# Kernel optimization log

Hardware: AMD Instinct MI355X
Metric: run time of the kernel (lower is better)

The kernel has to match this reference:

```python
import jax, jax.numpy as jnp
import numpy as np
import math
from jax import lax

A_BICUBIC = -0.75  # PyTorch bicubic coefficient


def _bicubic_resize_matrix(out_n, in_n):
    """Dense [out_n, in_n] matrix implementing 1D bicubic resize (half-pixel,
    align_corners=False, border-replicated taps) exactly like F.interpolate."""
    a = A_BICUBIC
    src = (np.arange(out_n) + 0.5) * (in_n / out_n) - 0.5
    i0 = np.floor(src).astype(np.int64)
    t = src - i0
    M = np.zeros((out_n, in_n), dtype=np.float32)
    for k in range(-1, 3):
        idx = np.clip(i0 + k, 0, in_n - 1)
        d = np.abs(t - k)
        w = np.where(d <= 1.0, (a + 2) * d**3 - (a + 3) * d**2 + 1.0,
                     np.where(d < 2.0, a * d**3 - 5 * a * d**2 + 8 * a * d - 4 * a, 0.0))
        np.add.at(M, (np.arange(out_n), idx), w)
    return jnp.asarray(M)


def _relative_position_index(w):
    coords = np.stack(np.meshgrid(np.arange(w), np.arange(w), indexing='ij'))  # [2,w,w]
    cf = coords.reshape(2, -1)
    rel = (cf[:, :, None] - cf[:, None, :]).transpose(1, 2, 0)  # [w^2,w^2,2]
    rel[..., 0] += w - 1
    rel[..., 1] += w - 1
    rel[..., 0] *= 2 * w - 1
    return rel.sum(-1)  # [w^2, w^2]


def _grid_sample_bilinear(img, grid):
    """img: [G,d,Hi,Wi]; grid: [G,Ho,Wo,2] (x,y) in [-1,1].
    Bilinear, padding_mode='zeros', align_corners=False."""
    G, d, Hi, Wi = img.shape
    Ho, Wo = grid.shape[1:3]
    gx = (grid[..., 0] + 1.0) * (Wi * 0.5) - 0.5
    gy = (grid[..., 1] + 1.0) * (Hi * 0.5) - 0.5
    x0 = jnp.floor(gx)
    y0 = jnp.floor(gy)
    imgf = img.reshape(G, d, Hi * Wi)
    out = jnp.zeros((G, d, Ho * Wo), img.dtype)
    for dy in (0, 1):
        for dx in (0, 1):
            xi = x0 + dx
            yi = y0 + dy
            w = (1.0 - jnp.abs(gx - xi)) * (1.0 - jnp.abs(gy - yi))
            valid = (xi >= 0) & (xi < Wi) & (yi >= 0) & (yi < Hi)
            xic = jnp.clip(xi, 0, Wi - 1).astype(jnp.int32)
            yic = jnp.clip(yi, 0, Hi - 1).astype(jnp.int32)
            flat = (yic * Wi + xic).reshape(G, 1, Ho * Wo)
            v = jnp.take_along_axis(imgf, flat, axis=2)  # [G,d,HoWo]
            out = out + v * (w * valid).reshape(G, 1, Ho * Wo)
    return out.reshape(G, d, Ho, Wo)


def deformable_attention(x, q_w, q_b, k_w, k_b, v_w, v_b, o_w, o_b, dw_w, dw_b, off_w, bias_table, offset_scale=2.0):
    B, N, C = x.shape
    H = W = int(math.sqrt(N))
    heads = off_w.shape[0] // 2
    hd = C // heads
    wsz = (int(math.isqrt(bias_table.shape[0])) + 1) // 2  # (2w-1)^2 -> w

    xi = x.reshape(B, H, W, C).transpose(0, 3, 1, 2)  # [B,C,H,W]

    def conv1x1(t, w, b=None):
        y = jnp.einsum('bchw,oc->bohw', t, w)
        return y if b is None else y + b[None, :, None, None]

    Q = conv1x1(xi, q_w, q_b)
    K = conv1x1(xi, k_w, k_b)
    V = conv1x1(xi, v_w, v_b)

    # offset network: depthwise 5x5 conv -> GELU -> 1x1 -> tanh -> *scale
    h = lax.conv_general_dilated(xi, dw_w, (1, 1), 'SAME', feature_group_count=C,
                                 dimension_numbers=('NCHW', 'OIHW', 'NCHW'))
    h = jax.nn.gelu(h + dw_b[None, :, None, None], approximate=False)
    offsets = jnp.tanh(conv1x1(h, off_w)) * offset_scale  # [B,2*heads,H,W]
    offsets = offsets.reshape(B, heads, 2, H, W).transpose(0, 1, 3, 4, 2)  # [B,n,H,W,2]

    gy, gx = jnp.meshgrid(jnp.linspace(-1.0, 1.0, H), jnp.linspace(-1.0, 1.0, W), indexing='ij')
    grid = jnp.stack((gx, gy), axis=-1)  # [H,W,2]
    samp = jnp.clip(grid[None, None] + offsets, -1.0, 1.0).reshape(B * heads, H, W, 2)

    Kh = K.reshape(B * heads, hd, H, W)
    Vh = V.reshape(B * heads, hd, H, W)
    Ks = _grid_sample_bilinear(Kh, samp).reshape(B, heads, hd, N).transpose(0, 1, 3, 2)  # [B,n,N,d]
    Vs = _grid_sample_bilinear(Vh, samp).reshape(B, heads, hd, N).transpose(0, 1, 3, 2)
    Qh = Q.reshape(B, heads, hd, N).transpose(0, 1, 3, 2)  # [B,n,N,d]

    scores = jnp.einsum('bhid,bhjd->bhij', Qh, Ks) / math.sqrt(hd)

    # relative bias: table lookup on static index, bicubic upsample w^2 -> N
    rpi = _relative_position_index(wsz)  # static numpy [w^2,w^2]
    bias0 = bias_table[jnp.asarray(rpi.reshape(-1)), 0].reshape(wsz * wsz, wsz * wsz)
    M = _bicubic_resize_matrix(N, wsz * wsz)
    bias = M @ bias0 @ M.T  # [N,N]
    scores = scores + bias[None, None]

    probs = jax.nn.softmax(scores, axis=-1)
    out = jnp.einsum('bhij,bhjd->bhid', probs, Vs)  # [B,n,N,d]
    out = out.transpose(0, 1, 3, 2).reshape(B, C, H, W)  # b (h d) p q
    out = conv1x1(out, o_w, o_b)
    return out.reshape(B, C, N).transpose(0, 2, 1)  # [B,N,C]


def setup_inputs() -> dict:
    key = jax.random.key(0)
    ks = jax.random.split(key, 16)
    B, N, C = 4, 1024, 512
    heads, wsz, kk = 8, 8, 5
    s = 0.02
    return {
        'x': jax.random.normal(ks[0], (B, N, C), jnp.float32),
        'q_w': jax.random.normal(ks[1], (C, C), jnp.float32) * s,
        'q_b': jax.random.normal(ks[2], (C,), jnp.float32) * s,
        'k_w': jax.random.normal(ks[3], (C, C), jnp.float32) * s,
        'k_b': jax.random.normal(ks[4], (C,), jnp.float32) * s,
        'v_w': jax.random.normal(ks[5], (C, C), jnp.float32) * s,
        'v_b': jax.random.normal(ks[6], (C,), jnp.float32) * s,
        'o_w': jax.random.normal(ks[7], (C, C), jnp.float32) * s,
        'o_b': jax.random.normal(ks[8], (C,), jnp.float32) * s,
        'dw_w': jax.random.normal(ks[9], (C, 1, kk, kk), jnp.float32) * s,
        'dw_b': jax.random.normal(ks[10], (C,), jnp.float32) * s,
        'off_w': jax.random.normal(ks[11], (2 * heads, C), jnp.float32) * s,
        'bias_table': jax.random.normal(ks[12], ((2 * wsz - 1) ** 2, 1), jnp.float32),
    }


def reference(x, q_w, q_b, k_w, k_b, v_w, v_b, o_w, o_b, dw_w, dw_b, off_w, bias_table):
    return deformable_attention(x, q_w, q_b, k_w, k_b, v_w, v_b, o_w, o_b, dw_w, dw_b, off_w, bias_table)
```

## Files before the change

### kernel.cpp

```cpp
#include <hip/hip_runtime.h>
#include <math.h>

typedef unsigned short ushort;
typedef __attribute__((ext_vector_type(8))) short bf16x8;
typedef __attribute__((ext_vector_type(4))) float f32x4;

#define MFMA16(a, b, c) __builtin_amdgcn_mfma_f32_16x16x32_bf16(a, b, c, 0, 0, 0)
#define GLOAD16(g, l)                                                   \
  __builtin_amdgcn_global_load_lds(                                     \
      (const __attribute__((address_space(1))) unsigned int*)(g),       \
      (__attribute__((address_space(3))) unsigned int*)(l), 16, 0, 0)

__device__ __forceinline__ ushort f2bf(float f) {
  unsigned u = __float_as_uint(f);
  u += 0x7FFFu + ((u >> 16) & 1u);
  return (ushort)(u >> 16);
}
__device__ __forceinline__ float bf2f(ushort b) {
  return __uint_as_float(((unsigned)b) << 16);
}
__device__ __forceinline__ unsigned pk_bf16(float a, float b) {
  unsigned u;
  asm("v_cvt_pk_bf16_f32 %0, %1, %2" : "=v"(u) : "v"(a), "v"(b));
  return u;
}

__device__ __forceinline__ void bicubic_taps(int i, float* w, int* idx) {
  const float a = -0.75f;
  float src = ((float)i + 0.5f) * 0.0625f - 0.5f;
  float fi = floorf(src);
  int i0 = (int)fi;
  float t = src - fi;
  #pragma unroll
  for (int k = -1; k <= 2; ++k) {
    float d = fabsf(t - (float)k);
    float wv;
    if (d <= 1.0f)
      wv = ((a + 2.0f) * d - (a + 3.0f)) * d * d + 1.0f;
    else if (d < 2.0f)
      wv = a * (((d - 5.0f) * d + 8.0f) * d - 4.0f);
    else
      wv = 0.0f;
    int ic = i0 + k;
    ic = ic < 0 ? 0 : (ic > 63 ? 63 : ic);
    w[k + 1] = wv;
    idx[k + 1] = ic;
  }
}

__global__ __launch_bounds__(256) void stage1(
    const float* __restrict__ x, const float* __restrict__ q_w,
    const float* __restrict__ k_w, const float* __restrict__ v_w,
    const float* __restrict__ o_w, const float* __restrict__ dw_w,
    const float* __restrict__ dw_b, const float* __restrict__ off_w,
    const float* __restrict__ btab, ushort* __restrict__ Xh,
    ushort* __restrict__ Wq, ushort* __restrict__ Wk, ushort* __restrict__ Wv,
    ushort* __restrict__ Woh, ushort* __restrict__ Wol,
    float* __restrict__ samp, ushort* __restrict__ biasb) {
  __shared__ float smem[16768];
  int blk = blockIdx.x;
  int tid = threadIdx.x;

  if (blk < 1024) {
    float* tab = smem;
    int i = blk;
    if (tid < 225) tab[tid] = btab[tid];
    __syncthreads();
    float wA[4]; int iA[4];
    bicubic_taps(i, wA, iA);
    for (int j = tid; j < 1024; j += 256) {
      float wB[4]; int iB[4];
      bicubic_taps(j, wB, iB);
      float sum = 0.f;
      #pragma unroll
      for (int ka = 0; ka < 4; ++ka) {
        int pa = iA[ka];
        int py = pa >> 3, px = pa & 7;
        float wa = wA[ka];
        #pragma unroll
        for (int kb = 0; kb < 4; ++kb) {
          int qb = iB[kb];
          int qy = qb >> 3, qx = qb & 7;
          sum += wa * wB[kb] * tab[(py - qy + 7) * 15 + (px - qx + 7)];
        }
      }
      biasb[(size_t)i * 1024 + j] = f2bf(sum);
    }
  } else if (blk < 1280) {
    float* wT = smem;
    float* hT = smem + 8256;
    float* ofs = smem + 16512;
    int ob = blk - 1024;
    int x0 = (ob & 1) * 16;
    int y = (ob >> 1) & 31;
    int b = ob >> 6;

    for (int e = tid; e < 2048; e += 256) {
      int o = e >> 7, c4 = e & 127;
      *(float4*)&wT[o * 516 + c4 * 4] = *(const float4*)&off_w[o * 512 + c4 * 4];
    }

    int c = tid * 2;
    float2 dwv[25];
    #pragma unroll
    for (int k = 0; k < 25; ++k) {
      dwv[k].x = dw_w[(size_t)c * 25 + k];
      dwv[k].y = dw_w[(size_t)(c + 1) * 25 + k];
    }
    float2 cb = *(const float2*)&dw_b[c];

    const float* xb = x + (size_t)b * 1024 * 512 + c;
    bool rv[5];
    #pragma unroll
    for (int r = 0; r < 5; ++r) {
      int yy = y - 2 + r;
      rv[r] = (yy >= 0 && yy < 32);
    }
    float2 win[5][5];
    #pragma unroll
    for (int j = 0; j < 4; ++j) {
      int xc = x0 - 2 + j;
      bool cvld = (xc >= 0 && xc < 32);
      #pragma unroll
      for (int r = 0; r < 5; ++r) {
        win[r][j] = (rv[r] && cvld)
            ? *(const float2*)&xb[(size_t)((y - 2 + r) * 32 + xc) * 512]
            : make_float2(0.f, 0.f);
      }
    }
    #pragma unroll
    for (int i = 0; i < 16; ++i) {
      int xc = x0 + i + 2;
      bool cvld = (xc < 32);
      #pragma unroll
      for (int r = 0; r < 5; ++r) {
        win[r][4] = (rv[r] && cvld)
            ? *(const float2*)&xb[(size_t)((y - 2 + r) * 32 + xc) * 512]
            : make_float2(0.f, 0.f);
      }
      float sx = cb.x, sy = cb.y;
      #pragma unroll
      for (int r = 0; r < 5; ++r)
        #pragma unroll
        for (int j = 0; j < 5; ++j) {
          sx += win[r][j].x * dwv[r * 5 + j].x;
          sy += win[r][j].y * dwv[r * 5 + j].y;
        }
      float g0 = 0.5f * sx * (1.0f + erff(sx * 0.70710678118654752f));
      float g1 = 0.5f * sy * (1.0f + erff(sy * 0.70710678118654752f));
      *(float2*)&hT[i * 516 + c] = make_float2(g0, g1);
      #pragma unroll
      for (int r = 0; r < 5; ++r) {
        win[r][0] = win[r][1]; win[r][1] = win[r][2];
        win[r][2] = win[r][3]; win[r][3] = win[r][4];
      }
    }
    __syncthreads();
    {
      int o = tid & 15, px = tid >> 4;
      float acc = 0.f;
      #pragma unroll 4
      for (int c4 = 0; c4 < 128; ++c4) {
        float4 hv = *(const float4*)&hT[px * 516 + c4 * 4];
        float4 wv = *(const float4*)&wT[o * 516 + c4 * 4];
        acc += hv.x * wv.x + hv.y * wv.y + hv.z * wv.z + hv.w * wv.w;
      }
      ofs[px * 16 + o] = tanhf(acc) * 2.0f;
    }
    __syncthreads();
    if (tid < 128) {
      int px = tid >> 3, h = tid & 7;
      int n = y * 32 + x0 + px;
      float gx = -1.0f + 2.0f * (float)(x0 + px) / 31.0f;
      float gy = -1.0f + 2.0f * (float)y / 31.0f;
      float sx = fminf(fmaxf(gx + ofs[px * 16 + 2 * h], -1.0f), 1.0f);
      float sy = fminf(fmaxf(gy + ofs[px * 16 + 2 * h + 1], -1.0f), 1.0f);
      float2 pc;
      pc.x = (sx + 1.0f) * 16.0f - 0.5f;
      pc.y = (sy + 1.0f) * 16.0f - 0.5f;
      ((float2*)samp)[(size_t)(b * 8 + h) * 1024 + n] = pc;
    }
  } else if (blk < 3328) {
    int i = (blk - 1280) * 256 + tid;
    float4 v = ((const float4*)x)[i];
    ushort4 h;
    h.x = f2bf(v.x); h.y = f2bf(v.y); h.z = f2bf(v.z); h.w = f2bf(v.w);
    ((ushort4*)Xh)[i] = h;
  } else {
    int blk2 = blk - 3328;
    int grp = blk2 >> 8;
    int i = (blk2 & 255) * 256 + tid;
    if (grp < 3) {
      const float* in = grp == 0 ? q_w : grp == 1 ? k_w : v_w;
      ushort* hi = grp == 0 ? Wq : grp == 1 ? Wk : Wv;
      float4 v = ((const float4*)in)[i];
      ushort4 h;
      h.x = f2bf(v.x); h.y = f2bf(v.y); h.z = f2bf(v.z); h.w = f2bf(v.w);
      ((ushort4*)hi)[i] = h;
    } else {
      float4 v = ((const float4*)o_w)[i];
      ushort4 h, l;
      h.x = f2bf(v.x); l.x = f2bf(v.x - bf2f(h.x));
      h.y = f2bf(v.y); l.y = f2bf(v.y - bf2f(h.y));
      h.z = f2bf(v.z); l.z = f2bf(v.z - bf2f(h.z));
      h.w = f2bf(v.w); l.w = f2bf(v.w - bf2f(h.w));
      ((ushort4*)Woh)[i] = h;
      ((ushort4*)Wol)[i] = l;
    }
  }
}

__global__ __launch_bounds__(256) void gemm_qkv(
    const ushort* __restrict__ X, const ushort* __restrict__ Wq,
    const ushort* __restrict__ Wk, const ushort* __restrict__ Wv,
    const float* __restrict__ b0, const float* __restrict__ b1,
    const float* __restrict__ b2, ushort* __restrict__ Qo,
    ushort* __restrict__ Ko, ushort* __restrict__ Vo) {
  __shared__ ushort lds[12288];
  ushort* sA = lds;
  ushort* sB = lds + 8192;
  int which = blockIdx.x >> 3;
  int n0 = (blockIdx.x & 7) * 64;
  int m0 = blockIdx.y * 128;
  const ushort* W; const float* bb; ushort* Y; float scale;
  if (which == 0)      { W = Wq; bb = b0; Y = Qo; scale = 0.125f; }
  else if (which == 1) { W = Wk; bb = b1; Y = Ko; scale = 1.0f; }
  else                 { W = Wv; bb = b2; Y = Vo; scale = 1.0f; }

  int tid = threadIdx.x;
  int lane = tid & 63;
  int w = tid >> 6;
  int wr = (w >> 1) * 64;
  int wc = (w & 1) * 32;
  int l8r = lane >> 3;
  int sll = ((lane & 7) ^ l8r) << 3;
  int l16 = lane & 15, lq = lane >> 4;

  f32x4 acc[4][2];
  f32x4 zero = {0.f, 0.f, 0.f, 0.f};
  #pragma unroll
  for (int m = 0; m < 4; ++m)
    #pragma unroll
    for (int n = 0; n < 2; ++n) acc[m][n] = zero;

  for (int kt = 0; kt < 8; ++kt) {
    int kk = kt * 64;
    __syncthreads();
    #pragma unroll
    for (int q = 0; q < 4; ++q) {
      int ci = w * 4 + q;
      GLOAD16(X + (size_t)(m0 + ci * 8 + l8r) * 512 + kk + sll, sA + ci * 512);
    }
    #pragma unroll
    for (int q = 0; q < 2; ++q) {
      int ci = w * 2 + q;
      GLOAD16(W + (size_t)(n0 + ci * 8 + l8r) * 512 + kk + sll, sB + ci * 512);
    }
    __syncthreads();
    #pragma unroll
    for (int ks = 0; ks < 2; ++ks) {
      int slot = ks * 4 + lq;
      bf16x8 a[4], bvv[2];
      #pragma unroll
      for (int m = 0; m < 4; ++m) {
        int r = wr + m * 16 + l16;
        a[m] = *(const bf16x8*)&sA[r * 64 + ((slot ^ (r & 7)) << 3)];
      }
      #pragma unroll
      for (int n = 0; n < 2; ++n) {
        int r = wc + n * 16 + l16;
        bvv[n] = *(const bf16x8*)&sB[r * 64 + ((slot ^ (r & 7)) << 3)];
      }
      #pragma unroll
      for (int m = 0; m < 4; ++m)
        #pragma unroll
        for (int n = 0; n < 2; ++n)
          acc[m][n] = MFMA16(a[m], bvv[n], acc[m][n]);
    }
  }
  #pragma unroll
  for (int n = 0; n < 2; ++n) {
    int col = n0 + wc + n * 16 + l16;
    float bv = bb[col];
    #pragma unroll
    for (int m = 0; m < 4; ++m) {
      #pragma unroll
      for (int j = 0; j < 4; ++j) {
        int row = m0 + wr + m * 16 + lq * 4 + j;
        Y[(size_t)row * 512 + col] = f2bf((acc[m][n][j] + bv) * scale);
      }
    }
  }
}

__global__ __launch_bounds__(256) void gemm_o(
    const ushort* __restrict__ A, const ushort* __restrict__ Wh,
    const ushort* __restrict__ Wl, const float* __restrict__ bias,
    float* __restrict__ Y) {
  __shared__ ushort sA[4096];
  __shared__ ushort sWh[4096];
  __shared__ ushort sWl[4096];
  int m0 = blockIdx.y * 64, n0 = blockIdx.x * 64;
  int tid = threadIdx.x;
  int lane = tid & 63;
  int w = tid >> 6;
  int wr = (w >> 1) * 32;
  int wc = (w & 1) * 32;
  int l8r = lane >> 3;
  int sll = ((lane & 7) ^ l8r) << 3;
  int l16 = lane & 15, lq = lane >> 4;

  f32x4 acc[2][2];
  f32x4 zero = {0.f, 0.f, 0.f, 0.f};
  #pragma unroll
  for (int m = 0; m < 2; ++m)
    #pragma unroll
    for (int n = 0; n < 2; ++n) acc[m][n] = zero;

  for (int kt = 0; kt < 8; ++kt) {
    int kk = kt * 64;
    __syncthreads();
    #pragma unroll
    for (int q = 0; q < 2; ++q) {
      int ci = w * 2 + q;
      size_t ga = (size_t)(m0 + ci * 8 + l8r) * 512 + kk + sll;
      GLOAD16(A + ga, sA + ci * 512);
      size_t gw = (size_t)(n0 + ci * 8 + l8r) * 512 + kk + sll;
      GLOAD16(Wh + gw, sWh + ci * 512);
      GLOAD16(Wl + gw, sWl + ci * 512);
    }
    __syncthreads();
    #pragma unroll
    for (int ks = 0; ks < 2; ++ks) {
      int slot = ks * 4 + lq;
      bf16x8 a[2], bh[2], bl[2];
      #pragma unroll
      for (int m = 0; m < 2; ++m) {
        int r = wr + m * 16 + l16;
        a[m] = *(const bf16x8*)&sA[r * 64 + ((slot ^ (r & 7)) << 3)];
      }
      #pragma unroll
      for (int n = 0; n < 2; ++n) {
        int r = wc + n * 16 + l16;
        int ph = (slot ^ (r & 7)) << 3;
        bh[n] = *(const bf16x8*)&sWh[r * 64 + ph];
        bl[n] = *(const bf16x8*)&sWl[r * 64 + ph];
      }
      #pragma unroll
      for (int m = 0; m < 2; ++m)
        #pragma unroll
        for (int n = 0; n < 2; ++n) {
          acc[m][n] = MFMA16(a[m], bh[n], acc[m][n]);
          acc[m][n] = MFMA16(a[m], bl[n], acc[m][n]);
        }
    }
  }
  #pragma unroll
  for (int n = 0; n < 2; ++n) {
    int col = n0 + wc + n * 16 + l16;
    float bv = bias[col];
    #pragma unroll
    for (int m = 0; m < 2; ++m) {
      #pragma unroll
      for (int j = 0; j < 4; ++j) {
        int row = m0 + wr + m * 16 + lq * 4 + j;
        Y[(size_t)row * 512 + col] = acc[m][n][j] + bv;
      }
    }
  }
}

__global__ __launch_bounds__(256) void grid_sample(
    const ushort* __restrict__ K, const ushort* __restrict__ V,
    const float* __restrict__ samp, ushort* __restrict__ Ks,
    ushort* __restrict__ Vt) {
  __shared__ ushort sV[64][72];
  int bh = blockIdx.y;
  int b = bh >> 3, h = bh & 7;
  int jb = blockIdx.x;
  int d = threadIdx.x & 63;
  for (int p = 0; p < 16; ++p) {
    int jl = p * 4 + (threadIdx.x >> 6);
    int j = jb * 64 + jl;
    float2 pc = ((const float2*)samp)[(size_t)bh * 1024 + j];
    float gx = pc.x, gy = pc.y;
    float x0 = floorf(gx), y0 = floorf(gy);
    float aK = 0.f, aV = 0.f;
    #pragma unroll
    for (int dy = 0; dy < 2; ++dy)
      #pragma unroll
      for (int dx = 0; dx < 2; ++dx) {
        float xi = x0 + (float)dx, yi = y0 + (float)dy;
        float wgt = (1.0f - fabsf(gx - xi)) * (1.0f - fabsf(gy - yi));
        if (xi >= 0.f && xi < 32.f && yi >= 0.f && yi < 32.f) {
          size_t base = ((size_t)b * 1024 + (int)yi * 32 + (int)xi) * 512 + h * 64 + d;
          aK += bf2f(K[base]) * wgt;
          aV += bf2f(V[base]) * wgt;
        }
      }
    Ks[((size_t)bh * 1024 + j) * 64 + d] = f2bf(aK);
    sV[jl][d] = f2bf(aV);
  }
  __syncthreads();
  int dd = threadIdx.x >> 2, c4 = threadIdx.x & 3;
  bf16x8 v0, v1;
  #pragma unroll
  for (int k = 0; k < 8; ++k) v0[k] = (short)sV[c4 * 16 + k][dd];
  #pragma unroll
  for (int k = 0; k < 8; ++k) v1[k] = (short)sV[c4 * 16 + 8 + k][dd];
  size_t o = ((size_t)bh * 64 + dd) * 1024 + jb * 64 + c4 * 16;
  *(bf16x8*)&Vt[o] = v0;
  *(bf16x8*)&Vt[o + 8] = v1;
}

__global__ __launch_bounds__(512, 6) void attn_mfma(
    const ushort* __restrict__ Qh, const ushort* __restrict__ Ks,
    const ushort* __restrict__ Vt, const ushort* __restrict__ bias,
    ushort* __restrict__ Oh) {
  __shared__ ushort sK[2][2][2048];
  __shared__ ushort sVt[2][2][2048];
  __shared__ ushort sP[8][640];

  int tid = threadIdx.x;
  int lane = tid & 63;
  int w = tid >> 6;
  int qg = w & 3;
  int kvh = w >> 2;
  int l16 = lane & 15, lq = lane >> 4;
  int blk = blockIdx.x;
  int xcd = blk & 7;
  int rr = blk >> 3;
  int bh = ((rr & 3) << 3) + xcd;
  int i0 = (rr >> 2) * 64;
  int b = bh >> 3, h = bh & 7;

  bf16x8 qh[2];
  #pragma unroll
  for (int s = 0; s < 2; ++s)
    qh[s] = *(const bf16x8*)&Qh[((size_t)b * 1024 + i0 + qg * 16 + l16) * 512 +
                                h * 64 + s * 32 + lq * 8];

  f32x4 oacc[4];
  f32x4 zero = {0.f, 0.f, 0.f, 0.f};
  #pragma unroll
  for (int n = 0; n < 4; ++n) oacc[n] = zero;
  float mq = -INFINITY, lsum = 0.f;

  ushort* myP = sP[w];
  int krow = qg * 8 + (lane >> 3);
  int kslot = (lane & 7) ^ (krow & 7);
  int vrow = qg * 16 + (lane >> 2);
  int vslot = (lane & 3) ^ (vrow & 3);
  size_t kbase = ((size_t)bh * 1024 + kvh * 512 + krow) * 64 + kslot * 8;
  size_t vbase = ((size_t)bh * 64 + vrow) * 1024 + kvh * 512 + vslot * 8;
  ushort* dK0 = &sK[0][kvh][qg * 8 * 64];  ushort* dK1 = &sK[1][kvh][qg * 8 * 64];
  ushort* dV0 = &sVt[0][kvh][qg * 16 * 32]; ushort* dV1 = &sVt[1][kvh][qg * 16 * 32];
  const ushort* bprow = bias + (size_t)(i0 + qg * 16 + l16) * 1024 + kvh * 512;

  GLOAD16(Ks + kbase, dK0);
  GLOAD16(Vt + vbase, dV0);
  ushort4 bias_c[2];
  #pragma unroll
  for (int n = 0; n < 2; ++n)
    bias_c[n] = *(const ushort4*)&bprow[n * 16 + lq * 4];
  __syncthreads();

  int cur = 0;
  for (int t = 0; t < 16; ++t) {
    if (t < 15) {
      size_t off = (size_t)(t + 1) * 32;
      GLOAD16(Ks + kbase + off * 64, cur ? dK0 : dK1);
      GLOAD16(Vt + vbase + off, cur ? dV0 : dV1);
    }
    f32x4 sacc[2];
    #pragma unroll
    for (int n = 0; n < 2; ++n) {
      sacc[n][0] = bf2f(bias_c[n].x);
      sacc[n][1] = bf2f(bias_c[n].y);
      sacc[n][2] = bf2f(bias_c[n].z);
      sacc[n][3] = bf2f(bias_c[n].w);
    }
    if (t < 15) {
      #pragma unroll
      for (int n = 0; n < 2; ++n)
        bias_c[n] = *(const ushort4*)&bprow[(t + 1) * 32 + n * 16 + lq * 4];
    }
    const ushort* k_t = sK[cur][kvh];
    __builtin_amdgcn_s_setprio(1);
    #pragma unroll
    for (int ks = 0; ks < 2; ++ks) {
      int cslot = ((ks * 4 + lq) ^ (l16 & 7)) * 8;
      #pragma unroll
      for (int n = 0; n < 2; ++n) {
        bf16x8 aK = *(const bf16x8*)&k_t[(n * 16 + l16) * 64 + cslot];
        sacc[n] = MFMA16(aK, qh[ks], sacc[n]);
      }
    }
    __builtin_amdgcn_s_setprio(0);
    float mt = fmaxf(fmaxf(fmaxf(sacc[0][0], sacc[0][1]), fmaxf(sacc[0][2], sacc[0][3])),
                     fmaxf(fmaxf(sacc[1][0], sacc[1][1]), fmaxf(sacc[1][2], sacc[1][3])));
    mt = fmaxf(mt, __shfl_xor(mt, 16));
    mt = fmaxf(mt, __shfl_xor(mt, 32));
    if (!__all(mt <= mq + 8.0f)) {
      float mn = fmaxf(mq, mt);
      float sc = __expf(mq - mn);
      mq = mn;
      lsum *= sc;
      float scq[4];
      #pragma unroll
      for (int r = 0; r < 4; ++r) scq[r] = __shfl(sc, lq * 4 + r);
      #pragma unroll
      for (int n = 0; n < 4; ++n)
        #pragma unroll
        for (int r = 0; r < 4; ++r) oacc[n][r] *= scq[r];
    }
    float ts = 0.f;
    #pragma unroll
    for (int n = 0; n < 2; ++n) {
      float p0 = __expf(sacc[n][0] - mq);
      float p1 = __expf(sacc[n][1] - mq);
      float p2 = __expf(sacc[n][2] - mq);
      float p3 = __expf(sacc[n][3] - mq);
      ts += (p0 + p1) + (p2 + p3);
      uint2 u = make_uint2(pk_bf16(p0, p1), pk_bf16(p2, p3));
      *(uint2*)&myP[l16 * 40 + n * 16 + lq * 4] = u;
    }
    ts += __shfl_xor(ts, 16);
    ts += __shfl_xor(ts, 32);
    lsum += ts;
    bf16x8 pa = *(const bf16x8*)&myP[l16 * 40 + lq * 8];
    const ushort* vt_t = sVt[cur][kvh];
    __builtin_amdgcn_s_setprio(1);
    #pragma unroll
    for (int n = 0; n < 4; ++n) {
      int row = n * 16 + l16;
      bf16x8 bv = *(const bf16x8*)&vt_t[row * 32 + ((lq ^ (row & 3)) * 8)];
      oacc[n] = MFMA16(pa, bv, oacc[n]);
    }
    __builtin_amdgcn_s_setprio(0);
    __syncthreads();
    cur ^= 1;
  }

  float* mO = (float*)sK;
  float* mML = (float*)sVt;
  if (w >= 4) {
    int base = ((w - 4) * 64 + lane) * 16;
    #pragma unroll
    for (int n = 0; n < 4; ++n)
      #pragma unroll
      for (int r = 0; r < 4; ++r) mO[base + n * 4 + r] = oacc[n][r];
    mML[((w - 4) * 64 + lane) * 2 + 0] = mq;
    mML[((w - 4) * 64 + lane) * 2 + 1] = lsum;
  }
  __syncthreads();
  if (w < 4) {
    float mB = mML[(w * 64 + lane) * 2 + 0];
    float lB = mML[(w * 64 + lane) * 2 + 1];
    float mS = fmaxf(mq, mB);
    float fA = __expf(mq - mS), fB = __expf(mB - mS);
    float linv = 1.0f / (lsum * fA + lB * fB);
    float cAv = fA * linv, cBv = fB * linv;
    float cA[4], cB[4];
    #pragma unroll
    for (int r = 0; r < 4; ++r) {
      cA[r] = __shfl(cAv, lq * 4 + r);
      cB[r] = __shfl(cBv, lq * 4 + r);
    }
    int base = (w * 64 + lane) * 16;
    #pragma unroll
    for (int r = 0; r < 4; ++r) {
      int qr = i0 + qg * 16 + lq * 4 + r;
      #pragma unroll
      for (int n = 0; n < 4; ++n) {
        float v = oacc[n][r] * cA[r] + mO[base + n * 4 + r] * cB[r];
        size_t o = ((size_t)b * 1024 + qr) * 512 + h * 64 + n * 16 + l16;
        Oh[o] = f2bf(v);
      }
    }
  }
}

extern "C" void kernel_launch(void* const* d_in, const int* in_sizes, int n_in,
                              void* d_out, int out_size, void* d_ws, size_t ws_size,
                              hipStream_t stream) {
  const float* x     = (const float*)d_in[0];
  const float* q_w   = (const float*)d_in[1];
  const float* q_b   = (const float*)d_in[2];
  const float* k_w   = (const float*)d_in[3];
  const float* k_b   = (const float*)d_in[4];
  const float* v_w   = (const float*)d_in[5];
  const float* v_b   = (const float*)d_in[6];
  const float* o_w   = (const float*)d_in[7];
  const float* o_b   = (const float*)d_in[8];
  const float* dw_w  = (const float*)d_in[9];
  const float* dw_b  = (const float*)d_in[10];
  const float* off_w = (const float*)d_in[11];
  const float* btab  = (const float*)d_in[12];

  float* ws = (float*)d_ws;
  const size_t SZ = (size_t)4 * 1024 * 512;
  float* samp = ws;

  ushort* u = (ushort*)(samp + 65536);
  ushort* Xh    = u;
  ushort* Qb    = Xh + SZ;
  ushort* Kb    = Qb + SZ;
  ushort* Vb    = Kb + SZ;
  ushort* Ksb   = Vb + SZ;
  ushort* Vtr   = Ksb + SZ;
  ushort* Aoh   = Vtr + SZ;
  ushort* biasb = Aoh + SZ;
  ushort* Wq    = biasb + 1048576;
  ushort* Wk    = Wq + 262144;
  ushort* Wv    = Wk + 262144;
  ushort* Woh   = Wv + 262144;
  ushort* Wol   = Woh + 262144;

  stage1<<<4352, 256, 0, stream>>>(x, q_w, k_w, v_w, o_w, dw_w, dw_b, off_w,
                                   btab, Xh, Wq, Wk, Wv, Woh, Wol, samp, biasb);

  gemm_qkv<<<dim3(24, 32), 256, 0, stream>>>(Xh, Wq, Wk, Wv, q_b, k_b, v_b,
                                             Qb, Kb, Vb);

  grid_sample<<<dim3(16, 32), 256, 0, stream>>>(Kb, Vb, samp, Ksb, Vtr);

  attn_mfma<<<512, 512, 0, stream>>>(Qb, Ksb, Vtr, biasb, Aoh);

  gemm_o<<<dim3(8, 64), 256, 0, stream>>>(Aoh, Woh, Wol, o_b, (float*)d_out);
}
```

Measured before the change: 103.6 us.

## Load attention K/V fragments directly from global and widen QKV GEMM tiles

The attention kernel drops the double-buffered LDS staging of K and V^T. Each wave now loads its MFMA operand fragments straight from global memory into registers, which removes the per-iteration block barrier and the LDS traffic. The loop is unrolled by four and the launch-bounds occupancy hint is lowered from six to four. Separately, the QKV GEMM moves to 512-thread blocks with 128x128 tiles, halving the grid and cutting redundant X loads. The risks are uncoalesced, duplicated global or L2 reads for K/V across query-group waves and fewer resident waves.

```diff
diff --git a/kernel.cpp b/kernel.cpp
--- a/kernel.cpp
+++ b/kernel.cpp
@@ -210,17 +210,17 @@
   }
 }
 
-__global__ __launch_bounds__(256) void gemm_qkv(
+__global__ __launch_bounds__(512) void gemm_qkv(
     const ushort* __restrict__ X, const ushort* __restrict__ Wq,
     const ushort* __restrict__ Wk, const ushort* __restrict__ Wv,
     const float* __restrict__ b0, const float* __restrict__ b1,
     const float* __restrict__ b2, ushort* __restrict__ Qo,
     ushort* __restrict__ Ko, ushort* __restrict__ Vo) {
-  __shared__ ushort lds[12288];
+  __shared__ ushort lds[16384];
   ushort* sA = lds;
   ushort* sB = lds + 8192;
-  int which = blockIdx.x >> 3;
-  int n0 = (blockIdx.x & 7) * 64;
+  int which = blockIdx.x >> 2;
+  int n0 = (blockIdx.x & 3) * 128;
   int m0 = blockIdx.y * 128;
   const ushort* W; const float* bb; ushort* Y; float scale;
   if (which == 0)      { W = Wq; bb = b0; Y = Qo; scale = 0.125f; }
@@ -230,8 +230,8 @@
   int tid = threadIdx.x;
   int lane = tid & 63;
   int w = tid >> 6;
-  int wr = (w >> 1) * 64;
-  int wc = (w & 1) * 32;
+  int wr = (w >> 2) * 64;
+  int wc = (w & 3) * 32;
   int l8r = lane >> 3;
   int sll = ((lane & 7) ^ l8r) << 3;
   int l16 = lane & 15, lq = lane >> 4;
@@ -247,13 +247,9 @@
     int kk = kt * 64;
     __syncthreads();
     #pragma unroll
-    for (int q = 0; q < 4; ++q) {
-      int ci = w * 4 + q;
-      GLOAD16(X + (size_t)(m0 + ci * 8 + l8r) * 512 + kk + sll, sA + ci * 512);
-    }
-    #pragma unroll
     for (int q = 0; q < 2; ++q) {
       int ci = w * 2 + q;
+      GLOAD16(X + (size_t)(m0 + ci * 8 + l8r) * 512 + kk + sll, sA + ci * 512);
       GLOAD16(W + (size_t)(n0 + ci * 8 + l8r) * 512 + kk + sll, sB + ci * 512);
     }
     __syncthreads();
@@ -413,13 +409,14 @@
   *(bf16x8*)&Vt[o + 8] = v1;
 }
 
-__global__ __launch_bounds__(512, 6) void attn_mfma(
+__global__ __launch_bounds__(512, 4) void attn_mfma(
     const ushort* __restrict__ Qh, const ushort* __restrict__ Ks,
     const ushort* __restrict__ Vt, const ushort* __restrict__ bias,
     ushort* __restrict__ Oh) {
-  __shared__ ushort sK[2][2][2048];
-  __shared__ ushort sVt[2][2][2048];
-  __shared__ ushort sP[8][640];
+  __shared__ char pool[18432];
+  ushort* sP = (ushort*)pool;
+  float* mO = (float*)pool;
+  float* mML = (float*)(pool + 16384);
 
   int tid = threadIdx.x;
   int lane = tid & 63;
@@ -446,56 +443,38 @@
   for (int n = 0; n < 4; ++n) oacc[n] = zero;
   float mq = -INFINITY, lsum = 0.f;
 
-  ushort* myP = sP[w];
-  int krow = qg * 8 + (lane >> 3);
-  int kslot = (lane & 7) ^ (krow & 7);
-  int vrow = qg * 16 + (lane >> 2);
-  int vslot = (lane & 3) ^ (vrow & 3);
-  size_t kbase = ((size_t)bh * 1024 + kvh * 512 + krow) * 64 + kslot * 8;
-  size_t vbase = ((size_t)bh * 64 + vrow) * 1024 + kvh * 512 + vslot * 8;
-  ushort* dK0 = &sK[0][kvh][qg * 8 * 64];  ushort* dK1 = &sK[1][kvh][qg * 8 * 64];
-  ushort* dV0 = &sVt[0][kvh][qg * 16 * 32]; ushort* dV1 = &sVt[1][kvh][qg * 16 * 32];
+  ushort* myP = sP + w * 640;
+  const ushort* Kp = Ks + ((size_t)bh * 1024 + kvh * 512 + l16) * 64 + lq * 8;
+  const ushort* Vp = Vt + ((size_t)bh * 64 + l16) * 1024 + kvh * 512 + lq * 8;
   const ushort* bprow = bias + (size_t)(i0 + qg * 16 + l16) * 1024 + kvh * 512;
 
-  GLOAD16(Ks + kbase, dK0);
-  GLOAD16(Vt + vbase, dV0);
-  ushort4 bias_c[2];
-  #pragma unroll
-  for (int n = 0; n < 2; ++n)
-    bias_c[n] = *(const ushort4*)&bprow[n * 16 + lq * 4];
-  __syncthreads();
-
-  int cur = 0;
+  #pragma unroll 4
   for (int t = 0; t < 16; ++t) {
-    if (t < 15) {
-      size_t off = (size_t)(t + 1) * 32;
-      GLOAD16(Ks + kbase + off * 64, cur ? dK0 : dK1);
-      GLOAD16(Vt + vbase + off, cur ? dV0 : dV1);
-    }
+    bf16x8 kf[2][2];
+    #pragma unroll
+    for (int ks = 0; ks < 2; ++ks)
+      #pragma unroll
+      for (int n = 0; n < 2; ++n)
+        kf[ks][n] = *(const bf16x8*)&Kp[(size_t)(t * 32 + n * 16) * 64 + ks * 32];
+    bf16x8 vf[4];
+    #pragma unroll
+    for (int n = 0; n < 4; ++n)
+      vf[n] = *(const bf16x8*)&Vp[(size_t)n * 16 * 1024 + t * 32];
     f32x4 sacc[2];
     #pragma unroll
     for (int n = 0; n < 2; ++n) {
-      sacc[n][0] = bf2f(bias_c[n].x);
-      sacc[n][1] = bf2f(bias_c[n].y);
-      sacc[n][2] = bf2f(bias_c[n].z);
-      sacc[n][3] = bf2f(bias_c[n].w);
-    }
-    if (t < 15) {
+      ushort4 bc = *(const ushort4*)&bprow[t * 32 + n * 16 + lq * 4];
+      sacc[n][0] = bf2f(bc.x);
+      sacc[n][1] = bf2f(bc.y);
+      sacc[n][2] = bf2f(bc.z);
+      sacc[n][3] = bf2f(bc.w);
+    }
+    __builtin_amdgcn_s_setprio(1);
+    #pragma unroll
+    for (int ks = 0; ks < 2; ++ks)
       #pragma unroll
       for (int n = 0; n < 2; ++n)
-        bias_c[n] = *(const ushort4*)&bprow[(t + 1) * 32 + n * 16 + lq * 4];
-    }
-    const ushort* k_t = sK[cur][kvh];
-    __builtin_amdgcn_s_setprio(1);
-    #pragma unroll
-    for (int ks = 0; ks < 2; ++ks) {
-      int cslot = ((ks * 4 + lq) ^ (l16 & 7)) * 8;
-      #pragma unroll
-      for (int n = 0; n < 2; ++n) {
-        bf16x8 aK = *(const bf16x8*)&k_t[(n * 16 + l16) * 64 + cslot];
-        sacc[n] = MFMA16(aK, qh[ks], sacc[n]);
-      }
-    }
+        sacc[n] = MFMA16(kf[ks][n], qh[ks], sacc[n]);
     __builtin_amdgcn_s_setprio(0);
     float mt = fmaxf(fmaxf(fmaxf(sacc[0][0], sacc[0][1]), fmaxf(sacc[0][2], sacc[0][3])),
                      fmaxf(fmaxf(sacc[1][0], sacc[1][1]), fmaxf(sacc[1][2], sacc[1][3])));
@@ -529,21 +508,13 @@
     ts += __shfl_xor(ts, 32);
     lsum += ts;
     bf16x8 pa = *(const bf16x8*)&myP[l16 * 40 + lq * 8];
-    const ushort* vt_t = sVt[cur][kvh];
     __builtin_amdgcn_s_setprio(1);
     #pragma unroll
-    for (int n = 0; n < 4; ++n) {
-      int row = n * 16 + l16;
-      bf16x8 bv = *(const bf16x8*)&vt_t[row * 32 + ((lq ^ (row & 3)) * 8)];
-      oacc[n] = MFMA16(pa, bv, oacc[n]);
-    }
+    for (int n = 0; n < 4; ++n) oacc[n] = MFMA16(pa, vf[n], oacc[n]);
     __builtin_amdgcn_s_setprio(0);
-    __syncthreads();
-    cur ^= 1;
-  }
-
-  float* mO = (float*)sK;
-  float* mML = (float*)sVt;
+  }
+
+  __syncthreads();
   if (w >= 4) {
     int base = ((w - 4) * 64 + lane) * 16;
     #pragma unroll
@@ -620,7 +591,7 @@
   stage1<<<4352, 256, 0, stream>>>(x, q_w, k_w, v_w, o_w, dw_w, dw_b, off_w,
                                    btab, Xh, Wq, Wk, Wv, Woh, Wol, samp, biasb);
 
-  gemm_qkv<<<dim3(24, 32), 256, 0, stream>>>(Xh, Wq, Wk, Wv, q_b, k_b, v_b,
+  gemm_qkv<<<dim3(12, 32), 512, 0, stream>>>(Xh, Wq, Wk, Wv, q_b, k_b, v_b,
                                              Qb, Kb, Vb);
 
   grid_sample<<<dim3(16, 32), 256, 0, stream>>>(Kb, Vb, samp, Ksb, Vtr);
```

Measured after the change: 154.2 us. 1.49x slower.
